# Performance work log

Measured on AMD Instinct MI355X. Metric: run time of the kernel, lower is better.

## Reference

```python
import jax, jax.numpy as jnp
import numpy as np
import math

T, B, D = 2048, 4, 1024
H, HD = 16, 64  # num_heads, head_dim


def _rope_cos_sin(t_len, head_dim):
    inv_freq = 1.0 / (10000.0 ** (jnp.arange(0, head_dim, 2, dtype=jnp.float32) / head_dim))
    t = jnp.arange(t_len, dtype=jnp.float32)
    freqs = jnp.einsum('i,j->ij', t, inv_freq)          # (T, HD/2)
    emb = jnp.concatenate([freqs, freqs], axis=-1)       # (T, HD)
    # broadcast over (T, B, H, HD)
    return jnp.cos(emb)[:, None, None, :], jnp.sin(emb)[:, None, None, :]


def _rotate_half(x):
    x1, x2 = jnp.split(x, 2, axis=-1)
    return jnp.concatenate([-x2, x1], axis=-1)


def setup_inputs() -> dict:
    key = jax.random.key(0)
    ks = jax.random.split(key, 5)
    x = jax.random.normal(ks[0], (T, B, D), dtype=jnp.float32)
    # causal mask: True = masked (future positions), shape (T, T)
    attention_mask = jnp.triu(jnp.ones((T, T), dtype=bool), k=1)
    W_qkv = jax.random.normal(ks[1], (3 * D, D), dtype=jnp.float32) * (1.0 / math.sqrt(D))
    b_qkv = jax.random.normal(ks[2], (3 * D,), dtype=jnp.float32) * 0.02
    W_out = jax.random.normal(ks[3], (D, D), dtype=jnp.float32) * (1.0 / math.sqrt(D))
    b_out = jax.random.normal(ks[4], (D,), dtype=jnp.float32) * 0.02
    return {"x": x, "attention_mask": attention_mask, "W_qkv": W_qkv,
            "b_qkv": b_qkv, "W_out": W_out, "b_out": b_out}


def reference(x, attention_mask, W_qkv, b_qkv, W_out, b_out):
    t_len, b_sz, d = x.shape
    qkv = x @ W_qkv.T + b_qkv                              # (T, B, 3D)
    q, k, v = jnp.split(qkv, 3, axis=-1)
    q = q.reshape(t_len, b_sz, H, HD)
    k = k.reshape(t_len, b_sz, H, HD)
    v = v.reshape(t_len, b_sz, H, HD)

    cos, sin = _rope_cos_sin(t_len, HD)
    q = q * cos + _rotate_half(q) * sin
    k = k * cos + _rotate_half(k) * sin

    scale = math.sqrt(HD)
    # scores: (B, H, T, S)
    scores = jnp.einsum('tbhd,sbhd->bhts', q, k) / scale
    scores = jnp.where(attention_mask[None, None, :, :], -jnp.inf, scores)
    probs = jax.nn.softmax(scores.astype(jnp.float32), axis=-1).astype(v.dtype)
    context = jnp.einsum('bhts,sbhd->tbhd', probs, v)      # (T, B, H, HD)
    context = context.reshape(t_len, b_sz, d)
    return context @ W_out.T + b_out
```

## Files before the change

### kernel.cpp

```cpp
#include <hip/hip_runtime.h>
#include <math.h>

#define T_LEN 2048
#define B_SZ 4
#define D_MODEL 1024
#define NH 16
#define HD 64
#define BH_TOT (B_SZ*NH)

typedef __attribute__((ext_vector_type(8))) short bf16x8;
typedef __attribute__((ext_vector_type(4))) float f32x4;
typedef __attribute__((ext_vector_type(16))) float f32x16;
typedef __attribute__((ext_vector_type(8))) unsigned short u16x8;
typedef __attribute__((ext_vector_type(4))) unsigned short u16x4;

union U8 { unsigned int u[4]; bf16x8 v; };

static __device__ __forceinline__ unsigned short f2bf(float f) {
  unsigned int x = __float_as_uint(f);
  x += 0x7fffu + ((x >> 16) & 1u);
  return (unsigned short)(x >> 16);
}
static __device__ __forceinline__ float bf2f(unsigned short u) {
  return __uint_as_float(((unsigned int)u) << 16);
}
static __device__ __forceinline__ void gload16(const void* g, void* l) {
  __builtin_amdgcn_global_load_lds((const __attribute__((address_space(1))) void*)g,
                                   (__attribute__((address_space(3))) void*)l, 16, 0, 0);
}

__global__ __launch_bounds__(256) void cvt3_kernel(
    const float* __restrict__ x, const float* __restrict__ wq, const float* __restrict__ wo,
    unsigned short* __restrict__ xb, unsigned short* __restrict__ wqb,
    unsigned short* __restrict__ wob) {
  const int i = blockIdx.x * 256 + threadIdx.x;
  const int N1 = T_LEN * B_SZ * D_MODEL / 8;
  const int N2 = N1 + 3 * D_MODEL * D_MODEL / 8;
  const int N3 = N2 + D_MODEL * D_MODEL / 8;
  const float* s; unsigned short* d; int off;
  if (i < N1)      { s = x;  d = xb;  off = i; }
  else if (i < N2) { s = wq; d = wqb; off = i - N1; }
  else if (i < N3) { s = wo; d = wob; off = i - N2; }
  else return;
  const float4 a = ((const float4*)s)[off * 2];
  const float4 b = ((const float4*)s)[off * 2 + 1];
  u16x8 o;
  o[0] = f2bf(a.x); o[1] = f2bf(a.y); o[2] = f2bf(a.z); o[3] = f2bf(a.w);
  o[4] = f2bf(b.x); o[5] = f2bf(b.y); o[6] = f2bf(b.z); o[7] = f2bf(b.w);
  ((u16x8*)d)[off] = o;
}

__global__ __launch_bounds__(256, 2) void gemm_mfma_kernel(
    const unsigned short* __restrict__ A, const unsigned short* __restrict__ W,
    const float* __restrict__ bias, float* __restrict__ C,
    int M, int N, int K, int mode,
    unsigned short* __restrict__ qd, unsigned short* __restrict__ kd,
    unsigned short* __restrict__ vtd)
{
  __shared__ unsigned short As[2][128 * 64];
  __shared__ unsigned short Bs[2][128 * 64];
  const int tid = threadIdx.x;
  const int l = tid & 63, w = tid >> 6;
  const int lq = l & 15, lg = l >> 4;
  const int wm = w >> 1, wn = w & 1;

  const int nbx = gridDim.x;
  const int nwg = nbx * gridDim.y;
  const int flat = blockIdx.y * nbx + blockIdx.x;
  const int cpx = nwg >> 3;
  const int swz = (flat & 7) * cpx + (flat >> 3);
  const int n0 = (swz % nbx) * 128, m0 = (swz / nbx) * 128;

  const int lrow = l >> 3;
  const int lcolb = ((l & 7) << 4) ^ (lrow << 4);

  f32x4 acc[4][4];
#pragma unroll
  for (int mt = 0; mt < 4; ++mt)
#pragma unroll
    for (int nt = 0; nt < 4; ++nt)
#pragma unroll
      for (int r2 = 0; r2 < 4; ++r2) acc[mt][nt][r2] = 0.f;

  const int nk = K >> 6;
#pragma unroll
  for (int c = 0; c < 4; ++c) {
    const int r0 = w * 32 + c * 8;
    const int row = r0 + lrow;
    gload16((const char*)A + ((size_t)(m0 + row) * K) * 2 + lcolb, (char*)As[0] + r0 * 128);
    gload16((const char*)W + ((size_t)(n0 + row) * K) * 2 + lcolb, (char*)Bs[0] + r0 * 128);
  }
  __syncthreads();

  for (int kt = 0; kt < nk; ++kt) {
    const int cur = kt & 1;
    if (kt + 1 < nk) {
      const int k1 = (kt + 1) << 6;
#pragma unroll
      for (int c = 0; c < 4; ++c) {
        const int r0 = w * 32 + c * 8;
        const int row = r0 + lrow;
        gload16((const char*)A + ((size_t)(m0 + row) * K + k1) * 2 + lcolb,
                (char*)As[cur ^ 1] + r0 * 128);
        gload16((const char*)W + ((size_t)(n0 + row) * K + k1) * 2 + lcolb,
                (char*)Bs[cur ^ 1] + r0 * 128);
      }
    }

#pragma unroll
    for (int kc = 0; kc < 2; ++kc) {
      bf16x8 af[4], bfr[4];
#pragma unroll
      for (int mt = 0; mt < 4; ++mt) {
        const int r = wm * 64 + mt * 16 + lq;
        af[mt] = *(const bf16x8*)((const char*)As[cur] + r * 128 +
                                  ((kc * 64 + lg * 16) ^ ((r & 7) << 4)));
      }
#pragma unroll
      for (int nt = 0; nt < 4; ++nt) {
        const int r = wn * 64 + nt * 16 + lq;
        bfr[nt] = *(const bf16x8*)((const char*)Bs[cur] + r * 128 +
                                   ((kc * 64 + lg * 16) ^ ((r & 7) << 4)));
      }
#pragma unroll
      for (int mt = 0; mt < 4; ++mt)
#pragma unroll
        for (int nt = 0; nt < 4; ++nt)
          acc[mt][nt] = __builtin_amdgcn_mfma_f32_16x16x32_bf16(af[mt], bfr[nt], acc[mt][nt], 0, 0, 0);
    }
    __syncthreads();
  }

  if (mode == 0) {
#pragma unroll
    for (int nt = 0; nt < 4; ++nt) {
      const int n = n0 + wn * 64 + nt * 16 + lq;
      const float bv = bias[n];
#pragma unroll
      for (int mt = 0; mt < 4; ++mt)
#pragma unroll
        for (int r2 = 0; r2 < 4; ++r2) {
          const int m = m0 + wm * 64 + mt * 16 + lg * 4 + r2;
          C[(size_t)m * N + n] = acc[mt][nt][r2] + bv;
        }
    }
  } else {
#pragma unroll
    for (int nt = 0; nt < 4; ++nt) {
      const int n = n0 + wn * 64 + nt * 16 + lq;
      const float bv = bias[n];
      const int which = n >> 10;
      const int h = (n >> 6) & (NH - 1);
      const int hd = n & 63;
#pragma unroll
      for (int mt = 0; mt < 4; ++mt)
#pragma unroll
        for (int r2 = 0; r2 < 4; ++r2) {
          const int m = m0 + wm * 64 + mt * 16 + lg * 4 + r2;
          const int t = m >> 2, b = m & 3;
          const unsigned short val = f2bf(acc[mt][nt][r2] + bv);
          if (which == 2) {
            vtd[((size_t)(b * NH + h) * HD + hd) * T_LEN + t] = val;
          } else {
            unsigned short* dst = (which == 0) ? qd : kd;
            dst[((size_t)(b * NH + h) * T_LEN + t) * HD + hd] = val;
          }
        }
    }
  }
}

__global__ void rope_bf16_kernel(unsigned short* __restrict__ qb, unsigned short* __restrict__ kb)
{
  const int idx = blockIdx.x * blockDim.x + threadIdx.x;
  const int i  = idx & 31;
  const int t  = (idx >> 5) & (T_LEN - 1);
  const int bh = idx >> 16;
  const float inv_freq = powf(10000.f, -(float)i / 32.f);
  float s, c;
  sincosf((float)t * inv_freq, &s, &c);
  const size_t base = ((size_t)bh * T_LEN + t) * HD;
  const float QS = 0.18033688011112042f;
  const float q1 = bf2f(qb[base + i]), q2 = bf2f(qb[base + i + 32]);
  qb[base + i]      = f2bf((q1 * c - q2 * s) * QS);
  qb[base + i + 32] = f2bf((q2 * c + q1 * s) * QS);
  const float k1 = bf2f(kb[base + i]), k2 = bf2f(kb[base + i + 32]);
  kb[base + i]      = f2bf(k1 * c - k2 * s);
  kb[base + i + 32] = f2bf(k2 * c + k1 * s);
}

__global__ __launch_bounds__(256, 3) void attn_mfma_kernel(
    const unsigned short* __restrict__ Qb,
    const unsigned short* __restrict__ Kb,
    const unsigned short* __restrict__ Vt,
    unsigned short* __restrict__ ctx)
{
  __shared__ unsigned short Ks[2][64 * 64];
  __shared__ unsigned short Vs[2][64 * 64];
  const int tid = threadIdx.x;
  const int l = tid & 63;
  const int w = tid >> 6;
  const int lq = l & 31;
  const int h = l >> 5;
  const int bh = blockIdx.x;
  const int qc = (T_LEN / 128 - 1) - blockIdx.y;
  const int b = bh >> 4, hh = bh & 15;
  const size_t tb = (size_t)bh * T_LEN;

  const int q0w = qc * 128 + w * 32;
  const int qg = q0w + lq;

  bf16x8 qf[4];
#pragma unroll
  for (int s = 0; s < 4; ++s)
    qf[s] = *(const bf16x8*)(Qb + (tb + qg) * HD + s * 16 + h * 8);

  f32x16 acc0, acc1;
#pragma unroll
  for (int r = 0; r < 16; ++r) { acc0[r] = 0.f; acc1[r] = 0.f; }
  float mrun = -1e30f, lsum = 0.f;

  const int lrow = l >> 3;
  const int lcolb = ((l & 7) << 4) ^ (lrow << 4);
  const int last = 2 * qc + 1;

#pragma unroll
  for (int c = 0; c < 2; ++c) {
    const int r0 = w * 16 + c * 8;
    const int row = r0 + lrow;
    gload16((const char*)Kb + ((tb + row) * HD) * 2 + lcolb, (char*)Ks[0] + r0 * 128);
    gload16((const char*)Vt + (((size_t)bh * HD + row) * T_LEN) * 2 + lcolb,
            (char*)Vs[0] + r0 * 128);
  }
  __syncthreads();

  for (int kbi = 0; kbi <= last; ++kbi) {
    const int s0 = kbi * 64;
    const int cur = kbi & 1;

    if (kbi < last) {
      const int sn = s0 + 64;
#pragma unroll
      for (int c = 0; c < 2; ++c) {
        const int r0 = w * 16 + c * 8;
        const int row = r0 + lrow;
        gload16((const char*)Kb + ((tb + sn + row) * HD) * 2 + lcolb,
                (char*)Ks[cur ^ 1] + r0 * 128);
        gload16((const char*)Vt + (((size_t)bh * HD + row) * T_LEN + sn) * 2 + lcolb,
                (char*)Vs[cur ^ 1] + r0 * 128);
      }
    }

    const int dmax = q0w + 31 - s0;
    if (dmax >= 0) {
      const char* Kc = (const char*)Ks[cur];
      const char* Vc = (const char*)Vs[cur];
      const bool st1 = (dmax >= 32);
      const bool maskN = (s0 + 63 > q0w);

      f32x16 sv0, sv1;
#pragma unroll
      for (int r = 0; r < 16; ++r) { sv0[r] = -1e30f; sv1[r] = -1e30f; }
      {
        f32x16 z;
#pragma unroll
        for (int r = 0; r < 16; ++r) z[r] = 0.f;
        const int krow = lq;
        const int kswz = (krow & 7) << 4;
        __builtin_amdgcn_s_setprio(1);
#pragma unroll
        for (int s = 0; s < 4; ++s) {
          bf16x8 ka = *(const bf16x8*)(Kc + krow * 128 + ((s * 32 + h * 16) ^ kswz));
          z = __builtin_amdgcn_mfma_f32_32x32x16_bf16(ka, qf[s], z, 0, 0, 0);
        }
        __builtin_amdgcn_s_setprio(0);
        sv0 = z;
      }
      if (st1) {
        f32x16 z;
#pragma unroll
        for (int r = 0; r < 16; ++r) z[r] = 0.f;
        const int krow = 32 + lq;
        const int kswz = (krow & 7) << 4;
        __builtin_amdgcn_s_setprio(1);
#pragma unroll
        for (int s = 0; s < 4; ++s) {
          bf16x8 ka = *(const bf16x8*)(Kc + krow * 128 + ((s * 32 + h * 16) ^ kswz));
          z = __builtin_amdgcn_mfma_f32_32x32x16_bf16(ka, qf[s], z, 0, 0, 0);
        }
        __builtin_amdgcn_s_setprio(0);
        sv1 = z;
      }

      if (maskN) {
#pragma unroll
        for (int r = 0; r < 16; ++r) {
          const int sl = (r & 3) + 8 * (r >> 2) + 4 * h;
          if (s0 + sl > qg)      sv0[r] = -1e30f;
          if (s0 + 32 + sl > qg) sv1[r] = -1e30f;
        }
      }

      float tmax = -1e30f;
#pragma unroll
      for (int r = 0; r < 16; ++r) tmax = fmaxf(tmax, fmaxf(sv0[r], sv1[r]));
      tmax = fmaxf(tmax, __shfl_xor(tmax, 32));
      const float mnew = fmaxf(mrun, tmax);
      const float alpha = exp2f(mrun - mnew);
      float ps = 0.f;
#pragma unroll
      for (int r = 0; r < 16; ++r) { sv0[r] = exp2f(sv0[r] - mnew); ps += sv0[r]; }
      if (st1) {
#pragma unroll
        for (int r = 0; r < 16; ++r) { sv1[r] = exp2f(sv1[r] - mnew); ps += sv1[r]; }
      }
      ps += __shfl_xor(ps, 32);
      lsum = lsum * alpha + ps;
      mrun = mnew;
#pragma unroll
      for (int r = 0; r < 16; ++r) { acc0[r] *= alpha; acc1[r] *= alpha; }

      unsigned int u0[4][2], u1[4][2];
#pragma unroll
      for (int a = 0; a < 4; ++a) {
        asm("v_cvt_pk_bf16_f32 %0, %1, %2" : "=v"(u0[a][0]) : "v"(sv0[4*a]),   "v"(sv0[4*a+1]));
        asm("v_cvt_pk_bf16_f32 %0, %1, %2" : "=v"(u0[a][1]) : "v"(sv0[4*a+2]), "v"(sv0[4*a+3]));
      }
      if (st1) {
#pragma unroll
        for (int a = 0; a < 4; ++a) {
          asm("v_cvt_pk_bf16_f32 %0, %1, %2" : "=v"(u1[a][0]) : "v"(sv1[4*a]),   "v"(sv1[4*a+1]));
          asm("v_cvt_pk_bf16_f32 %0, %1, %2" : "=v"(u1[a][1]) : "v"(sv1[4*a+2]), "v"(sv1[4*a+3]));
        }
      }

      const int vswz0 = (lq & 7) << 4;
#pragma unroll
      for (int st = 0; st < 2; ++st) {
        if (st == 1 && !st1) break;
#pragma unroll
        for (int cc = 0; cc < 2; ++cc) {
          unsigned int x0 = st ? u1[2*cc][0] : u0[2*cc][0];
          unsigned int y0 = st ? u1[2*cc+1][0] : u0[2*cc+1][0];
          unsigned int x1 = st ? u1[2*cc][1] : u0[2*cc][1];
          unsigned int y1 = st ? u1[2*cc+1][1] : u0[2*cc+1][1];
          asm("v_permlane32_swap_b32 %0, %1" : "+v"(x0), "+v"(y0));
          asm("v_permlane32_swap_b32 %0, %1" : "+v"(x1), "+v"(y1));
          U8 pf;
          pf.u[0] = x0; pf.u[1] = x1; pf.u[2] = y0; pf.u[3] = y1;
          const int soff = st * 64 + cc * 32 + h * 16;
          __builtin_amdgcn_s_setprio(1);
          {
            bf16x8 va = *(const bf16x8*)(Vc + lq * 128 + (soff ^ vswz0));
            acc0 = __builtin_amdgcn_mfma_f32_32x32x16_bf16(va, pf.v, acc0, 0, 0, 0);
          }
          {
            const int row = 32 + lq;
            bf16x8 va = *(const bf16x8*)(Vc + row * 128 + (soff ^ ((row & 7) << 4)));
            acc1 = __builtin_amdgcn_mfma_f32_32x32x16_bf16(va, pf.v, acc1, 0, 0, 0);
          }
          __builtin_amdgcn_s_setprio(0);
        }
      }
    }

    __syncthreads();
  }

  const float linv = 1.f / lsum;
  unsigned short* orow = ctx + ((size_t)qg * B_SZ + b) * D_MODEL + hh * HD;
#pragma unroll
  for (int g = 0; g < 4; ++g) {
    u16x4 o0, o1;
#pragma unroll
    for (int j = 0; j < 4; ++j) {
      o0[j] = f2bf(acc0[4*g + j] * linv);
      o1[j] = f2bf(acc1[4*g + j] * linv);
    }
    *(u16x4*)(orow + 8*g + 4*h)      = o0;
    *(u16x4*)(orow + 32 + 8*g + 4*h) = o1;
  }
}

extern "C" void kernel_launch(void* const* d_in, const int* in_sizes, int n_in,
                              void* d_out, int out_size, void* d_ws, size_t ws_size,
                              hipStream_t stream) {
  const float* x    = (const float*)d_in[0];
  const float* Wqkv = (const float*)d_in[2];
  const float* bqkv = (const float*)d_in[3];
  const float* Wout = (const float*)d_in[4];
  const float* bout = (const float*)d_in[5];
  float* out = (float*)d_out;

  char* wsb = (char*)d_ws;
  unsigned short* xb    = (unsigned short*)(wsb);
  unsigned short* wqkvb = (unsigned short*)(wsb + (16ull << 20));
  unsigned short* woutb = (unsigned short*)(wsb + (22ull << 20));
  unsigned short* qb    = (unsigned short*)(wsb + (24ull << 20));
  unsigned short* kb    = (unsigned short*)(wsb + (40ull << 20));
  unsigned short* vt    = (unsigned short*)(wsb + (56ull << 20));
  unsigned short* ctxb  = (unsigned short*)(wsb + (72ull << 20));

  const int ncvt = T_LEN*B_SZ*D_MODEL/8 + 3*D_MODEL*D_MODEL/8 + D_MODEL*D_MODEL/8;
  cvt3_kernel<<<(ncvt + 255)/256, 256, 0, stream>>>(x, Wqkv, Wout, xb, wqkvb, woutb);

  dim3 g1(3 * D_MODEL / 128, (T_LEN * B_SZ) / 128);
  gemm_mfma_kernel<<<g1, 256, 0, stream>>>(xb, wqkvb, bqkv, nullptr,
                                           T_LEN * B_SZ, 3 * D_MODEL, D_MODEL, 1,
                                           qb, kb, vt);
  const int rope_total = BH_TOT * T_LEN * (HD / 2);
  rope_bf16_kernel<<<(rope_total + 255) / 256, 256, 0, stream>>>(qb, kb);

  dim3 g2(BH_TOT, T_LEN / 128);
  attn_mfma_kernel<<<g2, 256, 0, stream>>>(qb, kb, vt, ctxb);

  dim3 g3(D_MODEL / 128, (T_LEN * B_SZ) / 128);
  gemm_mfma_kernel<<<g3, 256, 0, stream>>>(ctxb, woutb, bout, out,
                                           T_LEN * B_SZ, D_MODEL, D_MODEL, 0,
                                           nullptr, nullptr, nullptr);
}
```

Baseline: 220.3 us.

## Use 256x256 GEMM tiles with 8 waves and staggered async prefetch

```diff
diff --git a/kernel.cpp b/kernel.cpp
--- a/kernel.cpp
+++ b/kernel.cpp
@@ -50,85 +50,114 @@
   ((u16x8*)d)[off] = o;
 }
 
-__global__ __launch_bounds__(256, 2) void gemm_mfma_kernel(
+__global__ __launch_bounds__(512, 1) void gemm256_kernel(
     const unsigned short* __restrict__ A, const unsigned short* __restrict__ W,
     const float* __restrict__ bias, float* __restrict__ C,
     int M, int N, int K, int mode,
     unsigned short* __restrict__ qd, unsigned short* __restrict__ kd,
     unsigned short* __restrict__ vtd)
 {
-  __shared__ unsigned short As[2][128 * 64];
-  __shared__ unsigned short Bs[2][128 * 64];
+  __shared__ unsigned short As[2][256 * 64];
+  __shared__ unsigned short Bs[2][256 * 64];
   const int tid = threadIdx.x;
   const int l = tid & 63, w = tid >> 6;
   const int lq = l & 15, lg = l >> 4;
-  const int wm = w >> 1, wn = w & 1;
-
-  const int nbx = gridDim.x;
-  const int nwg = nbx * gridDim.y;
-  const int flat = blockIdx.y * nbx + blockIdx.x;
-  const int cpx = nwg >> 3;
-  const int swz = (flat & 7) * cpx + (flat >> 3);
-  const int n0 = (swz % nbx) * 128, m0 = (swz / nbx) * 128;
-
+  const int wm = w >> 2, wn = w & 3;
+  const int m0 = blockIdx.y * 256, n0 = blockIdx.x * 256;
   const int lrow = l >> 3;
   const int lcolb = ((l & 7) << 4) ^ (lrow << 4);
-
-  f32x4 acc[4][4];
-#pragma unroll
-  for (int mt = 0; mt < 4; ++mt)
+  const int nk = K >> 6;
+
+  auto stageA = [&](int t, int half) {
+    char* dst = (char*)As + (t & 1) * 32768 + half * 16384;
+    const size_t gr0 = (size_t)(m0 + half * 128);
+#pragma unroll
+    for (int c = 0; c < 2; ++c) {
+      const int seg = w * 2 + c;
+      const int row = seg * 8 + lrow;
+      gload16((const char*)A + ((gr0 + row) * (size_t)K + t * 64) * 2 + lcolb,
+              dst + seg * 1024);
+    }
+  };
+  auto stageB = [&](int t, int half) {
+    char* dst = (char*)Bs + (t & 1) * 32768 + half * 16384;
+    const size_t gr0 = (size_t)(n0 + half * 128);
+#pragma unroll
+    for (int c = 0; c < 2; ++c) {
+      const int seg = w * 2 + c;
+      const int row = seg * 8 + lrow;
+      gload16((const char*)W + ((gr0 + row) * (size_t)K + t * 64) * 2 + lcolb,
+              dst + seg * 1024);
+    }
+  };
+
+  f32x4 acc[8][4];
+#pragma unroll
+  for (int mt = 0; mt < 8; ++mt)
 #pragma unroll
     for (int nt = 0; nt < 4; ++nt)
 #pragma unroll
       for (int r2 = 0; r2 < 4; ++r2) acc[mt][nt][r2] = 0.f;
 
-  const int nk = K >> 6;
-#pragma unroll
-  for (int c = 0; c < 4; ++c) {
-    const int r0 = w * 32 + c * 8;
-    const int row = r0 + lrow;
-    gload16((const char*)A + ((size_t)(m0 + row) * K) * 2 + lcolb, (char*)As[0] + r0 * 128);
-    gload16((const char*)W + ((size_t)(n0 + row) * K) * 2 + lcolb, (char*)Bs[0] + r0 * 128);
-  }
-  __syncthreads();
-
-  for (int kt = 0; kt < nk; ++kt) {
-    const int cur = kt & 1;
-    if (kt + 1 < nk) {
-      const int k1 = (kt + 1) << 6;
-#pragma unroll
-      for (int c = 0; c < 4; ++c) {
-        const int r0 = w * 32 + c * 8;
-        const int row = r0 + lrow;
-        gload16((const char*)A + ((size_t)(m0 + row) * K + k1) * 2 + lcolb,
-                (char*)As[cur ^ 1] + r0 * 128);
-        gload16((const char*)W + ((size_t)(n0 + row) * K + k1) * 2 + lcolb,
-                (char*)Bs[cur ^ 1] + r0 * 128);
-      }
-    }
-
-#pragma unroll
-    for (int kc = 0; kc < 2; ++kc) {
-      bf16x8 af[4], bfr[4];
-#pragma unroll
-      for (int mt = 0; mt < 4; ++mt) {
-        const int r = wm * 64 + mt * 16 + lq;
-        af[mt] = *(const bf16x8*)((const char*)As[cur] + r * 128 +
-                                  ((kc * 64 + lg * 16) ^ ((r & 7) << 4)));
-      }
-#pragma unroll
-      for (int nt = 0; nt < 4; ++nt) {
-        const int r = wn * 64 + nt * 16 + lq;
-        bfr[nt] = *(const bf16x8*)((const char*)Bs[cur] + r * 128 +
-                                   ((kc * 64 + lg * 16) ^ ((r & 7) << 4)));
-      }
-#pragma unroll
-      for (int mt = 0; mt < 4; ++mt)
+  stageA(0, 0); stageA(0, 1);
+  stageB(0, 0); stageB(0, 1);
+  stageB(1, 0); stageB(1, 1);
+
+  for (int t = 0; t < nk; ++t) {
+    const int bsel = t & 1;
+    const char* Ac = (const char*)As + bsel * 32768;
+    const char* Bc = (const char*)Bs + bsel * 32768;
+
+    if (t < nk - 1) { asm volatile("s_waitcnt vmcnt(4)" ::: "memory"); }
+    else            { asm volatile("s_waitcnt vmcnt(0)" ::: "memory"); }
+    __builtin_amdgcn_s_barrier();
+    __builtin_amdgcn_sched_barrier(0);
+
+    bf16x8 bfr[4][2];
+#pragma unroll
+    for (int p = 0; p < 4; ++p) {
+      bf16x8 af[2][2];
+#pragma unroll
+      for (int i = 0; i < 2; ++i) {
+        const int r = wm * 128 + (2 * p + i) * 16 + lq;
+        const int x = (r & 7) << 4;
+#pragma unroll
+        for (int kc = 0; kc < 2; ++kc)
+          af[i][kc] = *(const bf16x8*)(Ac + r * 128 + ((kc * 64 + lg * 16) ^ x));
+      }
+      if (p == 0) {
+#pragma unroll
+        for (int nt = 0; nt < 4; ++nt) {
+          const int r = wn * 64 + nt * 16 + lq;
+          const int x = (r & 7) << 4;
+#pragma unroll
+          for (int kc = 0; kc < 2; ++kc)
+            bfr[nt][kc] = *(const bf16x8*)(Bc + r * 128 + ((kc * 64 + lg * 16) ^ x));
+        }
+      }
+
+      if (p == 0 && t + 1 < nk) stageA(t + 1, 0);
+      if (p == 1 && t + 1 < nk) stageA(t + 1, 1);
+      if (p == 2 && t + 2 < nk) stageB(t + 2, 0);
+      if (p == 3 && t + 2 < nk) stageB(t + 2, 1);
+
+      __builtin_amdgcn_s_setprio(1);
+#pragma unroll
+      for (int i = 0; i < 2; ++i)
 #pragma unroll
         for (int nt = 0; nt < 4; ++nt)
-          acc[mt][nt] = __builtin_amdgcn_mfma_f32_16x16x32_bf16(af[mt], bfr[nt], acc[mt][nt], 0, 0, 0);
-    }
-    __syncthreads();
+#pragma unroll
+          for (int kc = 0; kc < 2; ++kc)
+            acc[2 * p + i][nt] =
+                __builtin_amdgcn_mfma_f32_16x16x32_bf16(af[i][kc], bfr[nt][kc],
+                                                        acc[2 * p + i][nt], 0, 0, 0);
+      __builtin_amdgcn_s_setprio(0);
+
+      if (p < 3) {
+        __builtin_amdgcn_s_barrier();
+        __builtin_amdgcn_sched_barrier(0);
+      }
+    }
   }
 
   if (mode == 0) {
@@ -137,10 +166,10 @@
       const int n = n0 + wn * 64 + nt * 16 + lq;
       const float bv = bias[n];
 #pragma unroll
-      for (int mt = 0; mt < 4; ++mt)
+      for (int mt = 0; mt < 8; ++mt)
 #pragma unroll
         for (int r2 = 0; r2 < 4; ++r2) {
-          const int m = m0 + wm * 64 + mt * 16 + lg * 4 + r2;
+          const int m = m0 + wm * 128 + mt * 16 + lg * 4 + r2;
           C[(size_t)m * N + n] = acc[mt][nt][r2] + bv;
         }
     }
@@ -153,10 +182,10 @@
       const int h = (n >> 6) & (NH - 1);
       const int hd = n & 63;
 #pragma unroll
-      for (int mt = 0; mt < 4; ++mt)
+      for (int mt = 0; mt < 8; ++mt)
 #pragma unroll
         for (int r2 = 0; r2 < 4; ++r2) {
-          const int m = m0 + wm * 64 + mt * 16 + lg * 4 + r2;
+          const int m = m0 + wm * 128 + mt * 16 + lg * 4 + r2;
           const int t = m >> 2, b = m & 3;
           const unsigned short val = f2bf(acc[mt][nt][r2] + bv);
           if (which == 2) {
@@ -404,18 +433,18 @@
   const int ncvt = T_LEN*B_SZ*D_MODEL/8 + 3*D_MODEL*D_MODEL/8 + D_MODEL*D_MODEL/8;
   cvt3_kernel<<<(ncvt + 255)/256, 256, 0, stream>>>(x, Wqkv, Wout, xb, wqkvb, woutb);
 
-  dim3 g1(3 * D_MODEL / 128, (T_LEN * B_SZ) / 128);
-  gemm_mfma_kernel<<<g1, 256, 0, stream>>>(xb, wqkvb, bqkv, nullptr,
-                                           T_LEN * B_SZ, 3 * D_MODEL, D_MODEL, 1,
-                                           qb, kb, vt);
+  dim3 g1(3 * D_MODEL / 256, (T_LEN * B_SZ) / 256);
+  gemm256_kernel<<<g1, 512, 0, stream>>>(xb, wqkvb, bqkv, nullptr,
+                                         T_LEN * B_SZ, 3 * D_MODEL, D_MODEL, 1,
+                                         qb, kb, vt);
   const int rope_total = BH_TOT * T_LEN * (HD / 2);
   rope_bf16_kernel<<<(rope_total + 255) / 256, 256, 0, stream>>>(qb, kb);
 
   dim3 g2(BH_TOT, T_LEN / 128);
   attn_mfma_kernel<<<g2, 256, 0, stream>>>(qb, kb, vt, ctxb);
 
-  dim3 g3(D_MODEL / 128, (T_LEN * B_SZ) / 128);
-  gemm_mfma_kernel<<<g3, 256, 0, stream>>>(ctxb, woutb, bout, out,
-                                           T_LEN * B_SZ, D_MODEL, D_MODEL, 0,
-                                           nullptr, nullptr, nullptr);
-}
+  dim3 g3(D_MODEL / 256, (T_LEN * B_SZ) / 256);
+  gemm256_kernel<<<g3, 512, 0, stream>>>(ctxb, woutb, bout, out,
+                                         T_LEN * B_SZ, D_MODEL, D_MODEL, 0,
+                                         nullptr, nullptr, nullptr);
+}
```

New measurement: 236.5 us. 7.3% more time.
